# Performance work log

Hardware: AMD Instinct MI355X
Metric: run time of the kernel (lower is better)

## Reference

```python
import jax, jax.numpy as jnp
import numpy as np

N = 50000      # nodes
E = 800000     # edges per etype
IN, HID, OUT = 128, 128, 64
NH = 4         # heads in layerMH
NE = 2         # interaction edge types
NEG = 0.2      # GATConv leaky_relu negative slope


def _gat(x, src, dst, W, al, ar, b, heads, fdim):
    """DGL GATConv (residual=False, activation=None, bias=True).
    x: (N, in); W: (in, heads*fdim); al/ar: (heads, fdim); b: (heads*fdim,)
    Returns (N, heads, fdim)."""
    n = x.shape[0]
    z = (x @ W).reshape(n, heads, fdim)              # (N,H,F)
    el = jnp.sum(z * al, axis=-1)                    # (N,H)
    er = jnp.sum(z * ar, axis=-1)                    # (N,H)
    e = jax.nn.leaky_relu(el[src] + er[dst], NEG)    # (E,H)
    # edge softmax over incoming edges of each dst node
    m = jax.ops.segment_max(e, dst, num_segments=n)
    m = jnp.where(jnp.isfinite(m), m, 0.0)           # zero in-degree safety
    ex = jnp.exp(e - m[dst])
    den = jax.ops.segment_sum(ex, dst, num_segments=n)
    alpha = ex / jnp.maximum(den[dst], 1e-9)         # (E,H)
    out = jax.ops.segment_sum(alpha[:, :, None] * z[src], dst, num_segments=n)
    return out + b.reshape(1, heads, fdim)


def setup_inputs() -> dict:
    key = jax.random.key(0)
    ks = jax.random.split(key, 19)
    x = jax.random.normal(ks[0], (N, IN), jnp.float32)
    src0 = jax.random.randint(ks[1], (E,), 0, N, jnp.int32)
    dst0 = jax.random.randint(ks[2], (E,), 0, N, jnp.int32)
    src1 = jax.random.randint(ks[3], (E,), 0, N, jnp.int32)
    dst1 = jax.random.randint(ks[4], (E,), 0, N, jnp.int32)
    # per-etype GAT params (stacked over the NE edge types)
    W1 = jax.random.normal(ks[5], (NE, IN, HID), jnp.float32) / np.sqrt(IN)
    a_l1 = jax.random.normal(ks[6], (NE, 1, HID), jnp.float32) * 0.1
    a_r1 = jax.random.normal(ks[7], (NE, 1, HID), jnp.float32) * 0.1
    b1 = jnp.zeros((NE, HID), jnp.float32)
    W2 = jax.random.normal(ks[8], (NE, HID, OUT), jnp.float32) / np.sqrt(HID)
    a_l2 = jax.random.normal(ks[9], (NE, 1, OUT), jnp.float32) * 0.1
    a_r2 = jax.random.normal(ks[10], (NE, 1, OUT), jnp.float32) * 0.1
    b2 = jnp.zeros((NE, OUT), jnp.float32)
    Wm = jax.random.normal(ks[11], (NE, OUT, NH * OUT), jnp.float32) / np.sqrt(OUT)
    a_lm = jax.random.normal(ks[12], (NE, NH, OUT), jnp.float32) * 0.1
    a_rm = jax.random.normal(ks[13], (NE, NH, OUT), jnp.float32) * 0.1
    bm = jnp.zeros((NE, NH * OUT), jnp.float32)
    fc_w = jax.random.normal(ks[14], (NE, NE), jnp.float32) * (np.sqrt(2.0) / np.sqrt(NE))
    return dict(x=x, src0=src0, dst0=dst0, src1=src1, dst1=dst1,
                W1=W1, a_l1=a_l1, a_r1=a_r1, b1=b1,
                W2=W2, a_l2=a_l2, a_r2=a_r2, b2=b2,
                Wm=Wm, a_lm=a_lm, a_rm=a_rm, bm=bm, fc_w=fc_w)


def reference(x, src0, dst0, src1, dst1, W1, a_l1, a_r1, b1,
              W2, a_l2, a_r2, b2, Wm, a_lm, a_rm, bm, fc_w):
    srcs, dsts = (src0, src1), (dst0, dst1)
    # layer1: HeteroGraphConv mean over edge types, single head -> (N, HID)
    h1 = jnp.mean(jnp.stack([
        _gat(x, srcs[i], dsts[i], W1[i], a_l1[i], a_r1[i], b1[i], 1, HID)[:, 0, :]
        for i in range(NE)]), axis=0)
    # layer2: agg_func = fc over stacked etype axis, then mean -> (N, OUT)
    h2s = jnp.stack([
        _gat(h1, srcs[i], dsts[i], W2[i], a_l2[i], a_r2[i], b2[i], 1, OUT)[:, 0, :]
        for i in range(NE)], axis=-1)                       # (N, OUT, NE)
    h2 = jnp.mean(jnp.einsum('noe,fe->nof', h2s, fc_w), axis=-1)
    # multi-head layer: mean over edge types -> (N, NH, OUT)
    hm = jnp.mean(jnp.stack([
        _gat(h2, srcs[i], dsts[i], Wm[i], a_lm[i], a_rm[i], bm[i], NH, OUT)
        for i in range(NE)]), axis=0)
    # per-head mean-centering over nodes (vectorized over heads)
    return hm - jnp.mean(hm, axis=0, keepdims=True)
```

## Files before the change

kernel.cpp:

```cpp
#include <hip/hip_runtime.h>

#define NN 50000
#define EE 800000

using short8v = __attribute__((ext_vector_type(8))) short;
using f32x4 = __attribute__((ext_vector_type(4))) float;

__device__ inline unsigned int bf_pack(float lo, float hi) {
  unsigned int a = __float_as_uint(lo);
  a += 0x7FFFu + ((a >> 16) & 1u);
  unsigned int b = __float_as_uint(hi);
  b += 0x7FFFu + ((b >> 16) & 1u);
  return (a >> 16) | ((b >> 16) << 16);
}
__device__ inline void bf_dec8(uint4 v, float* f) {
  f[0] = __uint_as_float(v.x << 16); f[1] = __uint_as_float(v.x & 0xFFFF0000u);
  f[2] = __uint_as_float(v.y << 16); f[3] = __uint_as_float(v.y & 0xFFFF0000u);
  f[4] = __uint_as_float(v.z << 16); f[5] = __uint_as_float(v.z & 0xFFFF0000u);
  f[6] = __uint_as_float(v.w << 16); f[7] = __uint_as_float(v.w & 0xFFFF0000u);
}
__device__ inline float lrelu(float v) { return v >= 0.f ? v : 0.2f * v; }

__device__ inline void split_pack8(const float* v, uint4& h, uint4& l) {
  unsigned int hb[8], lb[8];
  #pragma unroll
  for (int j = 0; j < 8; j++) {
    unsigned int b = __float_as_uint(v[j]);
    hb[j] = b & 0xFFFF0000u;
    float r = v[j] - __uint_as_float(hb[j]);
    lb[j] = __float_as_uint(r) & 0xFFFF0000u;
  }
  h.x = (hb[0] >> 16) | hb[1]; h.y = (hb[2] >> 16) | hb[3];
  h.z = (hb[4] >> 16) | hb[5]; h.w = (hb[6] >> 16) | hb[7];
  l.x = (lb[0] >> 16) | lb[1]; l.y = (lb[2] >> 16) | lb[3];
  l.z = (lb[4] >> 16) | lb[5]; l.w = (lb[6] >> 16) | lb[7];
}

#define SC_BPR 256

__global__ __launch_bounds__(256) void fold_k(
    const float* __restrict__ W1, const float* __restrict__ al1, const float* __restrict__ ar1,
    const float* __restrict__ W2, const float* __restrict__ al2, const float* __restrict__ ar2,
    const float* __restrict__ Wm, const float* __restrict__ alm, const float* __restrict__ arm,
    float* __restrict__ wl1, float* __restrict__ wr1,
    float* __restrict__ wl2, float* __restrict__ wr2,
    float* __restrict__ wlm, float* __restrict__ wrm) {
  int t = blockIdx.x * 256 + threadIdx.x;
  if (t < 512) {
    int lr = t >> 8, e = (t >> 7) & 1, k = t & 127;
    const float* a = (lr ? ar1 : al1) + e * 128;
    const float* w = W1 + ((size_t)e * 128 + k) * 128;
    float s = 0.f;
    for (int f = 0; f < 128; f++) s += w[f] * a[f];
    (lr ? wr1 : wl1)[e * 128 + k] = s;
  } else if (t < 1024) {
    int u = t - 512;
    int lr = u >> 8, e = (u >> 7) & 1, k = u & 127;
    const float* a = (lr ? ar2 : al2) + e * 64;
    const float* w = W2 + ((size_t)e * 128 + k) * 64;
    float s = 0.f;
    for (int f = 0; f < 64; f++) s += w[f] * a[f];
    (lr ? wr2 : wl2)[e * 128 + k] = s;
  } else if (t < 2048) {
    int u = t - 1024;
    int lr = u >> 9, e = (u >> 8) & 1, h = (u >> 6) & 3, k = u & 63;
    const float* a = (lr ? arm : alm) + (e * 4 + h) * 64;
    const float* w = Wm + ((size_t)e * 64 + k) * 256 + h * 64;
    float s = 0.f;
    for (int f = 0; f < 64; f++) s += w[f] * a[f];
    (lr ? wrm : wlm)[(e * 4 + h) * 64 + k] = s;
  }
}

__global__ __launch_bounds__(256) void front_k(
    const int* __restrict__ dst0, const int* __restrict__ dst1,
    int* __restrict__ deg, int* __restrict__ rel,
    const float* __restrict__ x, const float* __restrict__ wl,
    const float* __restrict__ wr, unsigned int* __restrict__ xb,
    float* __restrict__ el, float* __restrict__ er,
    const float* __restrict__ W1, const float* __restrict__ W2,
    const float* __restrict__ Wm,
    unsigned short* __restrict__ w1h, unsigned short* __restrict__ w1l,
    unsigned short* __restrict__ w2h, unsigned short* __restrict__ w2l,
    unsigned short* __restrict__ wmh, unsigned short* __restrict__ wml) {
  const int blk = blockIdx.x;
  if (blk < 1563) {
    int i = blk * 256 + threadIdx.x;
    if (i < 200000) {
      int4 d = ((const int4*)dst0)[i];
      int4 r;
      r.x = atomicAdd(&deg[d.x], 1);
      r.y = atomicAdd(&deg[d.y], 1);
      r.z = atomicAdd(&deg[d.z], 1);
      r.w = atomicAdd(&deg[d.w], 1);
      ((int4*)rel)[i] = r;
    } else if (i < 400000) {
      int4 d = ((const int4*)dst1)[i - 200000];
      int* dg = deg + 50000;
      int4 r;
      r.x = atomicAdd(&dg[d.x], 1);
      r.y = atomicAdd(&dg[d.y], 1);
      r.z = atomicAdd(&dg[d.z], 1);
      r.w = atomicAdd(&dg[d.w], 1);
      ((int4*)(rel + EE))[i - 200000] = r;
    }
  } else if (blk < 4688) {
    int bx = blk - 1563;
    int n = bx * 16 + (threadIdx.x >> 4);
    int lane = threadIdx.x & 15;
    if (n >= NN) return;
    float p[4] = {0.f, 0.f, 0.f, 0.f};
    #pragma unroll
    for (int i = 0; i < 2; i++) {
      int c = (lane + i * 16) * 4;
      float4 xv = *(const float4*)(x + (size_t)n * 128 + c);
      uint2 o;
      o.x = bf_pack(xv.x, xv.y);
      o.y = bf_pack(xv.z, xv.w);
      *(uint2*)(xb + (size_t)n * 64 + c / 2) = o;
      #pragma unroll
      for (int e = 0; e < 2; e++) {
        float4 a = *(const float4*)(wl + e * 128 + c);
        float4 b = *(const float4*)(wr + e * 128 + c);
        p[e*2+0] += xv.x*a.x + xv.y*a.y + xv.z*a.z + xv.w*a.w;
        p[e*2+1] += xv.x*b.x + xv.y*b.y + xv.z*b.z + xv.w*b.w;
      }
    }
    #pragma unroll
    for (int off = 1; off < 16; off <<= 1) {
      #pragma unroll
      for (int i = 0; i < 4; i++) p[i] += __shfl_xor(p[i], off);
    }
    if (lane == 0) {
      el[n] = p[0]; er[n] = p[1];
      el[NN + n] = p[2]; er[NN + n] = p[3];
    }
  } else {
    int t = (blk - 4688) * 256 + threadIdx.x;
    float v; unsigned short *ph, *pl; int oi;
    if (t < 32768) {
      int j = t & 7, n = (t >> 3) & 127, kg = (t >> 10) & 15, e = t >> 14;
      v = W1[((size_t)(e * 128 + kg * 8 + j)) * 128 + n];
      ph = w1h; pl = w1l; oi = t;
    } else if (t < 49152) {
      int i = t - 32768;
      int j = i & 7, n = (i >> 3) & 63, kg = (i >> 9) & 15, e = i >> 13;
      v = W2[((size_t)(e * 128 + kg * 8 + j)) * 64 + n];
      ph = w2h; pl = w2l; oi = i;
    } else if (t < 81920) {
      int i = t - 49152;
      int j = i & 7, n = (i >> 3) & 255, kg = (i >> 11) & 7, e = i >> 14;
      v = Wm[((size_t)(e * 64 + kg * 8 + j)) * 256 + n];
      ph = wmh; pl = wml; oi = i;
    } else return;
    unsigned int b = __float_as_uint(v);
    unsigned int hb = b & 0xFFFF0000u;
    float r = v - __uint_as_float(hb);
    unsigned int lb = __float_as_uint(r);
    ph[oi] = (unsigned short)(hb >> 16);
    pl[oi] = (unsigned short)(lb >> 16);
  }
}

__global__ __launch_bounds__(512) void scan1_k(const int* __restrict__ deg,
                                               int* __restrict__ inc,
                                               int* __restrict__ bsum) {
  __shared__ int s[512];
  int e = blockIdx.y;
  int t = threadIdx.x, i = blockIdx.x * 512 + t;
  int v = (i < NN) ? deg[e * 50000 + i] : 0;
  s[t] = v; __syncthreads();
  #pragma unroll
  for (int off = 1; off < 512; off <<= 1) {
    int u = (t >= off) ? s[t - off] : 0;
    __syncthreads();
    s[t] += u;
    __syncthreads();
  }
  if (i < NN) inc[e * 50000 + i] = s[t];
  if (t == 511) bsum[e * 128 + blockIdx.x] = s[511];
}

__global__ __launch_bounds__(128) void scan2_k(int* __restrict__ bsum, int nb) {
  __shared__ int s[128];
  int e = blockIdx.x;
  int t = threadIdx.x;
  int v = (t < nb) ? bsum[e * 128 + t] : 0;
  s[t] = v; __syncthreads();
  #pragma unroll
  for (int off = 1; off < 128; off <<= 1) {
    int u = (t >= off) ? s[t - off] : 0;
    __syncthreads();
    s[t] += u;
    __syncthreads();
  }
  if (t < nb) bsum[e * 128 + t] = s[t] - v;
}

__global__ __launch_bounds__(256) void scan3_k(const int* __restrict__ deg,
                                               const int* __restrict__ inc,
                                               const int* __restrict__ bsum,
                                               int* __restrict__ rowptr) {
  int e = blockIdx.y;
  int i = blockIdx.x * 256 + threadIdx.x;
  if (i < NN) {
    rowptr[e * 50001 + i] =
        inc[e * 50000 + i] - deg[e * 50000 + i] + bsum[e * 128 + (i >> 9)];
  }
  if (i == NN) rowptr[e * 50001 + NN] = EE;
}

__global__ __launch_bounds__(256) void passB_k(
    const int* __restrict__ src0, const int* __restrict__ dst0,
    const int* __restrict__ src1, const int* __restrict__ dst1,
    const int* __restrict__ rel, const int* __restrict__ rowptr,
    int* __restrict__ csr_src) {
  __shared__ int rp_s[2][6250];
  const int range = blockIdx.x & 7;
  const int bpr = blockIdx.x >> 3;
  const int lo = range * 6250;
  const int hi = lo + 6250;
  for (int k = threadIdx.x; k < 6250; k += 256) {
    rp_s[0][k] = rowptr[lo + k];
    rp_s[1][k] = rowptr[50001 + lo + k];
  }
  __syncthreads();
  #pragma unroll
  for (int e = 0; e < 2; e++) {
    const int4* ds4 = (const int4*)(e ? dst1 : dst0);
    const int* ss = e ? src1 : src0;
    const int4* rl4 = (const int4*)(rel + (size_t)e * EE);
    const int* rps = rp_s[e];
    int* outp = csr_src + (size_t)e * EE;
    for (int i = bpr * 256 + threadIdx.x; i < EE / 4; i += SC_BPR * 256) {
      int4 d = ds4[i];
      int4 rl = rl4[i];
      int b = i * 4;
      if (d.x >= lo && d.x < hi) outp[rps[d.x - lo] + rl.x] = ss[b];
      if (d.y >= lo && d.y < hi) outp[rps[d.y - lo] + rl.y] = ss[b + 1];
      if (d.z >= lo && d.z < hi) outp[rps[d.z - lo] + rl.z] = ss[b + 2];
      if (d.w >= lo && d.w < hi) outp[rps[d.w - lo] + rl.w] = ss[b + 3];
    }
  }
}

__global__ __launch_bounds__(256) void agg_x_f(
    const int* __restrict__ rowptr, const int* __restrict__ csr_src,
    const float* __restrict__ el, const float* __restrict__ er,
    const uint4* __restrict__ xb, float* __restrict__ u1) {
  int d = blockIdx.x * 16 + (threadIdx.x >> 4);
  int lane = threadIdx.x & 15;
  if (d >= NN) return;
  const int e = blockIdx.y;
  const int* rp = rowptr + e * 50001;
  const int* cs = csr_src + (size_t)e * EE;
  const float* elp = el + (size_t)e * NN;
  float erd = er[(size_t)e * NN + d];
  int j0 = rp[d], j1 = rp[d + 1];
  float sm = 0.f;
  float acc[8] = {};
  for (int j = j0; j < j1; j += 16) {
    int cnt = j1 - j; if (cnt > 16) cnt = 16;
    int jj = j + (lane < cnt ? lane : 0);
    int sl = cs[jj];
    float alv = (lane < cnt) ? __expf(lrelu(elp[sl] + erd)) : 0.f;
    sm += alv;
    {
      int sv[8]; float av[8]; uint4 xv[8];
      #pragma unroll
      for (int k = 0; k < 8; k++) {
        sv[k] = __shfl(sl, k, 16);
        av[k] = __shfl(alv, k, 16);
      }
      #pragma unroll
      for (int k = 0; k < 8; k++) xv[k] = xb[(size_t)sv[k] * 16 + lane];
      #pragma unroll
      for (int k = 0; k < 8; k++) {
        float f[8]; bf_dec8(xv[k], f);
        #pragma unroll
        for (int c = 0; c < 8; c++) acc[c] += av[k] * f[c];
      }
    }
    if (cnt > 8) {
      int sv[8]; float av[8]; uint4 xv[8];
      #pragma unroll
      for (int k = 0; k < 8; k++) {
        sv[k] = __shfl(sl, 8 + k, 16);
        av[k] = __shfl(alv, 8 + k, 16);
      }
      #pragma unroll
      for (int k = 0; k < 8; k++) xv[k] = xb[(size_t)sv[k] * 16 + lane];
      #pragma unroll
      for (int k = 0; k < 8; k++) {
        float f[8]; bf_dec8(xv[k], f);
        #pragma unroll
        for (int c = 0; c < 8; c++) acc[c] += av[k] * f[c];
      }
    }
  }
  #pragma unroll
  for (int off = 1; off < 16; off <<= 1) sm += __shfl_xor(sm, off, 16);
  float inv = 1.f / fmaxf(sm, 1e-9f);
  float* up = u1 + ((size_t)e * NN + d) * 128 + lane * 8;
  *(float4*)up       = make_float4(acc[0]*inv, acc[1]*inv, acc[2]*inv, acc[3]*inv);
  *(float4*)(up + 4) = make_float4(acc[4]*inv, acc[5]*inv, acc[6]*inv, acc[7]*inv);
}

__global__ __launch_bounds__(256) void layer12_k(
    const float* __restrict__ u1, const unsigned short* __restrict__ w1h,
    const unsigned short* __restrict__ w1l, const float* __restrict__ b1,
    const unsigned short* __restrict__ w2h, const unsigned short* __restrict__ w2l,
    const float* __restrict__ wl2, const float* __restrict__ wr2,
    unsigned int* __restrict__ Zb, float* __restrict__ el,
    float* __restrict__ er) {
  __shared__ float smem[64 * 132];
  uint4* AsH = (uint4*)smem;
  uint4* AsL = AsH + 256;
  float* Hs = smem;
  const int tid = threadIdx.x;
  const int row0 = blockIdx.x * 64;
  const int wv = tid >> 6, lane = tid & 63;
  const int l15 = lane & 15, lg = lane >> 4;
  const uint4* b1h4 = (const uint4*)w1h;
  const uint4* b1l4 = (const uint4*)w1l;
  const uint4* b2h4 = (const uint4*)w2h;
  const uint4* b2l4 = (const uint4*)w2l;

  f32x4 acc[8] = {};
  for (int e = 0; e < 2; e++) {
    const float* Ap = u1 + (size_t)e * NN * 128;
    for (int k0 = 0; k0 < 128; k0 += 32) {
      {
        int r = tid & 63, kgl = tid >> 6;
        int rr = row0 + r; if (rr >= NN) rr = NN - 1;
        const float* ap = Ap + (size_t)rr * 128 + k0 + kgl * 8;
        float4 a0 = *(const float4*)ap;
        float4 a1 = *(const float4*)(ap + 4);
        float v[8] = {a0.x, a0.y, a0.z, a0.w, a1.x, a1.y, a1.z, a1.w};
        uint4 hh, ll;
        split_pack8(v, hh, ll);
        AsH[kgl * 64 + r] = hh;
        AsL[kgl * 64 + r] = ll;
      }
      __syncthreads();
      int slot = lg * 64 + wv * 16 + l15;
      short8v ah = *reinterpret_cast<const short8v*>(&AsH[slot]);
      short8v al = *reinterpret_cast<const short8v*>(&AsL[slot]);
      int kgb = e * 16 + (k0 >> 3) + lg;
      #pragma unroll
      for (int nf = 0; nf < 8; nf++) {
        int bslot = kgb * 128 + nf * 16 + l15;
        short8v bh = *reinterpret_cast<const short8v*>(&b1h4[bslot]);
        short8v bl = *reinterpret_cast<const short8v*>(&b1l4[bslot]);
        acc[nf] = __builtin_amdgcn_mfma_f32_16x16x32_bf16(ah, bh, acc[nf], 0, 0, 0);
        acc[nf] = __builtin_amdgcn_mfma_f32_16x16x32_bf16(al, bh, acc[nf], 0, 0, 0);
        acc[nf] = __builtin_amdgcn_mfma_f32_16x16x32_bf16(ah, bl, acc[nf], 0, 0, 0);
      }
      __syncthreads();
    }
  }
  #pragma unroll
  for (int nf = 0; nf < 8; nf++) {
    int col = nf * 16 + l15;
    float bb = 0.5f * (b1[col] + b1[128 + col]);
    #pragma unroll
    for (int reg = 0; reg < 4; reg++) {
      int rloc = wv * 16 + lg * 4 + reg;
      Hs[rloc * 132 + col] = 0.5f * acc[nf][reg] + bb;
    }
  }
  __syncthreads();
  {
    int r = tid >> 2, q = tid & 3;
    int grow = row0 + r;
    const float* hrow = Hs + r * 132;
    float p0 = 0.f, p1 = 0.f, p2 = 0.f, p3 = 0.f;
    #pragma unroll 8
    for (int c = 0; c < 32; c++) {
      int k = q + c * 4;
      float hv = hrow[k];
      p0 += hv * wl2[k];       p1 += hv * wr2[k];
      p2 += hv * wl2[128 + k]; p3 += hv * wr2[128 + k];
    }
    p0 += __shfl_xor(p0, 1); p0 += __shfl_xor(p0, 2);
    p1 += __shfl_xor(p1, 1); p1 += __shfl_xor(p1, 2);
    p2 += __shfl_xor(p2, 1); p2 += __shfl_xor(p2, 2);
    p3 += __shfl_xor(p3, 1); p3 += __shfl_xor(p3, 2);
    if (q == 0 && grow < NN) {
      el[grow] = p0;      er[grow] = p1;
      el[NN + grow] = p2; er[NN + grow] = p3;
    }
  }
  f32x4 acc2[2][4] = {};
  for (int k0 = 0; k0 < 128; k0 += 32) {
    int ra = wv * 16 + l15;
    const float* hp = Hs + ra * 132 + k0 + lg * 8;
    float4 h0 = *(const float4*)hp;
    float4 h1v = *(const float4*)(hp + 4);
    float v[8] = {h0.x, h0.y, h0.z, h0.w, h1v.x, h1v.y, h1v.z, h1v.w};
    uint4 hh, ll;
    split_pack8(v, hh, ll);
    short8v ah = *reinterpret_cast<const short8v*>(&hh);
    short8v al = *reinterpret_cast<const short8v*>(&ll);
    #pragma unroll
    for (int e = 0; e < 2; e++) {
      int kgb = e * 16 + (k0 >> 3) + lg;
      #pragma unroll
      for (int nf = 0; nf < 4; nf++) {
        int bslot = kgb * 64 + nf * 16 + l15;
        short8v bh = *reinterpret_cast<const short8v*>(&b2h4[bslot]);
        short8v bl = *reinterpret_cast<const short8v*>(&b2l4[bslot]);
        acc2[e][nf] = __builtin_amdgcn_mfma_f32_16x16x32_bf16(ah, bh, acc2[e][nf], 0, 0, 0);
        acc2[e][nf] = __builtin_amdgcn_mfma_f32_16x16x32_bf16(al, bh, acc2[e][nf], 0, 0, 0);
        acc2[e][nf] = __builtin_amdgcn_mfma_f32_16x16x32_bf16(ah, bl, acc2[e][nf], 0, 0, 0);
      }
    }
  }
  #pragma unroll
  for (int e = 0; e < 2; e++) {
    #pragma unroll
    for (int nf = 0; nf < 4; nf++) {
      #pragma unroll
      for (int reg = 0; reg < 4; reg++) {
        float v = acc2[e][nf][reg];
        float nb = __shfl_xor(v, 1);
        int row = row0 + wv * 16 + lg * 4 + reg;
        if (!(lane & 1) && row < NN) {
          Zb[((size_t)e * NN + row) * 32 + nf * 8 + (l15 >> 1)] = bf_pack(v, nb);
        }
      }
    }
  }
}

__global__ __launch_bounds__(256) void agg2_f(
    const int* __restrict__ rowptr, const int* __restrict__ csr_src,
    const float* __restrict__ el, const float* __restrict__ er,
    const uint4* __restrict__ zb, const float* __restrict__ bias,
    const float* __restrict__ fcw, const float* __restrict__ wlm,
    const float* __restrict__ wrm, uint4* __restrict__ h2b,
    float* __restrict__ elm, float* __restrict__ erm) {
  int d = blockIdx.x * 32 + (threadIdx.x >> 3);
  int lane = threadIdx.x & 7;
  if (d >= NN) return;
  int c0 = lane * 8;
  float coef0 = 0.5f * (fcw[0] + fcw[2]);
  float coef1 = 0.5f * (fcw[1] + fcw[3]);
  float hrow[8];
  #pragma unroll
  for (int c = 0; c < 8; c++)
    hrow[c] = coef0 * bias[c0 + c] + coef1 * bias[64 + c0 + c];
  #pragma unroll
  for (int e = 0; e < 2; e++) {
    const int* rp = rowptr + e * 50001;
    const int* cs = csr_src + (size_t)e * EE;
    const float* elp = el + (size_t)e * NN;
    float erd = er[(size_t)e * NN + d];
    const uint4* zp = zb + (size_t)e * NN * 8;
    int j0 = rp[d], j1 = rp[d + 1];
    float sm = 0.f;
    float acc[8] = {};
    for (int j = j0; j < j1; j += 8) {
      int cnt = j1 - j; if (cnt > 8) cnt = 8;
      int jj = j + (lane < cnt ? lane : 0);
      int sl = cs[jj];
      float alv = (lane < cnt) ? __expf(lrelu(elp[sl] + erd)) : 0.f;
      sm += alv;
      int sv[8]; float av[8]; uint4 zv[8];
      #pragma unroll
      for (int k = 0; k < 8; k++) {
        sv[k] = __shfl(sl, k, 8);
        av[k] = __shfl(alv, k, 8);
      }
      #pragma unroll
      for (int k = 0; k < 8; k++) zv[k] = zp[(size_t)sv[k] * 8 + lane];
      #pragma unroll
      for (int k = 0; k < 8; k++) {
        float f[8]; bf_dec8(zv[k], f);
        #pragma unroll
        for (int c = 0; c < 8; c++) acc[c] += av[k] * f[c];
      }
    }
    #pragma unroll
    for (int off = 1; off < 8; off <<= 1) sm += __shfl_xor(sm, off, 8);
    float cinv = (e ? coef1 : coef0) / fmaxf(sm, 1e-9f);
    #pragma unroll
    for (int c = 0; c < 8; c++) hrow[c] += cinv * acc[c];
  }
  uint4 o;
  o.x = bf_pack(hrow[0], hrow[1]); o.y = bf_pack(hrow[2], hrow[3]);
  o.z = bf_pack(hrow[4], hrow[5]); o.w = bf_pack(hrow[6], hrow[7]);
  h2b[(size_t)d * 8 + lane] = o;
  float p[16];
  #pragma unroll
  for (int e2 = 0; e2 < 2; e2++) {
    #pragma unroll
    for (int h = 0; h < 4; h++) {
      const float* a = wlm + (e2 * 4 + h) * 64 + c0;
      const float* b = wrm + (e2 * 4 + h) * 64 + c0;
      float sl = 0.f, sr = 0.f;
      #pragma unroll
      for (int c = 0; c < 8; c++) { sl += hrow[c] * a[c]; sr += hrow[c] * b[c]; }
      p[e2*4+h] = sl; p[8+e2*4+h] = sr;
    }
  }
  #pragma unroll
  for (int off = 1; off < 8; off <<= 1) {
    #pragma unroll
    for (int i = 0; i < 16; i++) p[i] += __shfl_xor(p[i], off, 8);
  }
  if (lane == 0) *(float4*)(elm + (size_t)d * 4)        = make_float4(p[0], p[1], p[2], p[3]);
  if (lane == 1) *(float4*)(elm + ((size_t)NN + d) * 4) = make_float4(p[4], p[5], p[6], p[7]);
  if (lane == 2) *(float4*)(erm + (size_t)d * 4)        = make_float4(p[8], p[9], p[10], p[11]);
  if (lane == 3) *(float4*)(erm + ((size_t)NN + d) * 4) = make_float4(p[12], p[13], p[14], p[15]);
}

__global__ __launch_bounds__(256) void agg_mh_k(
    const int* __restrict__ rowptr, const int* __restrict__ csr_src,
    const float* __restrict__ elm, const float* __restrict__ erm,
    const uint4* __restrict__ h2b, float* __restrict__ u) {
  int d = blockIdx.x * 32 + (threadIdx.x >> 3);
  int lane = threadIdx.x & 7, c0 = lane * 8;
  if (d >= NN) return;
  const int e = blockIdx.y;
  const int* rp = rowptr + e * 50001;
  const int* cs = csr_src + (size_t)e * EE;
  const float* elp = elm + (size_t)e * NN * 4;
  float4 er4 = *(const float4*)(erm + ((size_t)e * NN + d) * 4);
  int j0 = rp[d], j1 = rp[d + 1];
  float4 sm = make_float4(0.f, 0.f, 0.f, 0.f);
  float acc[4][8] = {};
  for (int j = j0; j < j1; j += 4) {
    int cnt = j1 - j; if (cnt > 4) cnt = 4;
    int sq[4];
    #pragma unroll
    for (int q = 0; q < 4; q++) sq[q] = cs[j + (q < cnt ? q : 0)];
    float4 vq[4]; uint4 hq[4];
    #pragma unroll
    for (int q = 0; q < 4; q++) vq[q] = *(const float4*)(elp + (size_t)sq[q] * 4);
    #pragma unroll
    for (int q = 0; q < 4; q++) hq[q] = h2b[(size_t)sq[q] * 8 + lane];
    #pragma unroll
    for (int q = 0; q < 4; q++) {
      float g = (q < cnt) ? 1.f : 0.f;
      float4 w;
      w.x = g * __expf(lrelu(vq[q].x + er4.x));
      w.y = g * __expf(lrelu(vq[q].y + er4.y));
      w.z = g * __expf(lrelu(vq[q].z + er4.z));
      w.w = g * __expf(lrelu(vq[q].w + er4.w));
      sm.x += w.x; sm.y += w.y; sm.z += w.z; sm.w += w.w;
      float f[8]; bf_dec8(hq[q], f);
      #pragma unroll
      for (int c = 0; c < 8; c++) {
        acc[0][c] += w.x * f[c];
        acc[1][c] += w.y * f[c];
        acc[2][c] += w.z * f[c];
        acc[3][c] += w.w * f[c];
      }
    }
  }
  float4 inv = make_float4(1.f / fmaxf(sm.x, 1e-9f), 1.f / fmaxf(sm.y, 1e-9f),
                           1.f / fmaxf(sm.z, 1e-9f), 1.f / fmaxf(sm.w, 1e-9f));
  float iv[4] = {inv.x, inv.y, inv.z, inv.w};
  #pragma unroll
  for (int h = 0; h < 4; h++) {
    float* up = u + (((size_t)(e * 4 + h) * NN) + d) * 64 + c0;
    *(float4*)up       = make_float4(acc[h][0]*iv[h], acc[h][1]*iv[h],
                                     acc[h][2]*iv[h], acc[h][3]*iv[h]);
    *(float4*)(up + 4) = make_float4(acc[h][4]*iv[h], acc[h][5]*iv[h],
                                     acc[h][6]*iv[h], acc[h][7]*iv[h]);
  }
}

__global__ __launch_bounds__(256) void colsum_u_k(
    const float* __restrict__ u, float* __restrict__ usum) {
  __shared__ float lds[4][64];
  int eh = blockIdx.x >> 6;
  int chunk = blockIdx.x & 63;
  int c = threadIdx.x & 63, rg = threadIdx.x >> 6;
  const float* up = u + (size_t)eh * NN * 64;
  int n0 = chunk * 782;
  int n1 = n0 + 782; if (n1 > NN) n1 = NN;
  float s = 0.f;
  for (int n = n0 + rg; n < n1; n += 4) s += up[(size_t)n * 64 + c];
  lds[rg][c] = s;
  __syncthreads();
  if (rg == 0) {
    float t = lds[0][c] + lds[1][c] + lds[2][c] + lds[3][c];
    unsafeAtomicAdd(&usum[eh * 64 + c], t);
  }
}

__global__ __launch_bounds__(256) void mean_k(
    const float* __restrict__ usum, const float* __restrict__ Wm,
    float* __restrict__ mean) {
  int c = threadIdx.x;
  int h = c >> 6;
  float s = 0.f;
  for (int e = 0; e < 2; e++) {
    const float* us = usum + (e * 4 + h) * 64;
    const float* wp = Wm + (size_t)e * 64 * 256 + c;
    for (int k = 0; k < 64; k++) s += us[k] * wp[(size_t)k * 256];
  }
  mean[c] = s * (0.5f / NN);
}

__global__ __launch_bounds__(256) void out_gemm_k(
    const float* __restrict__ u, const unsigned short* __restrict__ wmh,
    const unsigned short* __restrict__ wml, const float* __restrict__ mean,
    float* __restrict__ out) {
  __shared__ uint4 AsH[512], AsL[512];
  const int h = blockIdx.y;
  const int tid = threadIdx.x;
  const int row0 = blockIdx.x * 128;
  const int wv = tid >> 6, lane = tid & 63;
  const int l15 = lane & 15, lg = lane >> 4;
  f32x4 acc[2][4] = {};
  const uint4* bh4 = (const uint4*)wmh;
  const uint4* bl4 = (const uint4*)wml;
  for (int e = 0; e < 2; e++) {
    const float* Ap = u + (size_t)(e * 4 + h) * NN * 64;
    for (int k0 = 0; k0 < 64; k0 += 32) {
      {
        int r = tid & 127, half = tid >> 7;
        int rr = row0 + r; if (rr >= NN) rr = NN - 1;
        const float* ap = Ap + (size_t)rr * 64 + k0;
        #pragma unroll
        for (int i = 0; i < 2; i++) {
          int kg = half * 2 + i;
          float4 a0 = *(const float4*)(ap + kg * 8);
          float4 a1 = *(const float4*)(ap + kg * 8 + 4);
          float v[8] = {a0.x, a0.y, a0.z, a0.w, a1.x, a1.y, a1.z, a1.w};
          uint4 hh, ll;
          split_pack8(v, hh, ll);
          AsH[kg * 128 + r] = hh;
          AsL[kg * 128 + r] = ll;
        }
      }
      __syncthreads();
      short8v ah[2], al[2];
      #pragma unroll
      for (int mf = 0; mf < 2; mf++) {
        int slot = lg * 128 + wv * 32 + mf * 16 + l15;
        ah[mf] = *reinterpret_cast<const short8v*>(&AsH[slot]);
        al[mf] = *reinterpret_cast<const short8v*>(&AsL[slot]);
      }
      int kgb = e * 8 + (k0 >> 3) + lg;
      #pragma unroll
      for (int nf = 0; nf < 4; nf++) {
        int bslot = kgb * 256 + h * 64 + nf * 16 + l15;
        short8v bh = *reinterpret_cast<const short8v*>(&bh4[bslot]);
        short8v bl = *reinterpret_cast<const short8v*>(&bl4[bslot]);
        #pragma unroll
        for (int mf = 0; mf < 2; mf++) {
          acc[mf][nf] = __builtin_amdgcn_mfma_f32_16x16x32_bf16(ah[mf], bh, acc[mf][nf], 0, 0, 0);
          acc[mf][nf] = __builtin_amdgcn_mfma_f32_16x16x32_bf16(al[mf], bh, acc[mf][nf], 0, 0, 0);
          acc[mf][nf] = __builtin_amdgcn_mfma_f32_16x16x32_bf16(ah[mf], bl, acc[mf][nf], 0, 0, 0);
        }
      }
      __syncthreads();
    }
  }
  #pragma unroll
  for (int nf = 0; nf < 4; nf++) {
    int col = nf * 16 + l15;
    float mn = mean[h * 64 + col];
    #pragma unroll
    for (int mf = 0; mf < 2; mf++) {
      #pragma unroll
      for (int reg = 0; reg < 4; reg++) {
        int row = row0 + wv * 32 + mf * 16 + lg * 4 + reg;
        if (row < NN)
          out[(size_t)row * 256 + h * 64 + col] = 0.5f * acc[mf][nf][reg] - mn;
      }
    }
  }
}

extern "C" void kernel_launch(void* const* d_in, const int* in_sizes, int n_in,
                              void* d_out, int out_size, void* d_ws, size_t ws_size,
                              hipStream_t stream) {
  const float* x  = (const float*)d_in[0];
  const int* src0 = (const int*)d_in[1];
  const int* dst0 = (const int*)d_in[2];
  const int* src1 = (const int*)d_in[3];
  const int* dst1 = (const int*)d_in[4];
  const float* W1  = (const float*)d_in[5];
  const float* al1 = (const float*)d_in[6];
  const float* ar1 = (const float*)d_in[7];
  const float* b1  = (const float*)d_in[8];
  const float* W2  = (const float*)d_in[9];
  const float* al2 = (const float*)d_in[10];
  const float* ar2 = (const float*)d_in[11];
  const float* b2  = (const float*)d_in[12];
  const float* Wm  = (const float*)d_in[13];
  const float* alm = (const float*)d_in[14];
  const float* arm = (const float*)d_in[15];
  const float* fcw = (const float*)d_in[17];
  float* out = (float*)d_out;

  float* ws = (float*)d_ws;
  float* zu     = ws;
  unsigned int* z2b = (unsigned int*)(ws + 12800000);
  unsigned int* xb = (unsigned int*)(ws + 25600000);
  unsigned int* h2b = (unsigned int*)(ws + 32000000);
  float* el     = ws + 33600000;
  float* er     = ws + 34000000;
  float* elm    = ws + 34400000;
  float* erm    = ws + 34800000;
  float* wl1    = ws + 35200000;
  float* wr1    = wl1 + 256;
  float* wl2    = wr1 + 256;
  float* wr2    = wl2 + 256;
  float* wlm    = wr2 + 256;
  float* wrm    = wlm + 512;
  float* usum   = wrm + 512;
  float* meanp  = usum + 512;
  int* rowptr  = (int*)(meanp + 256);
  int* csr_src = rowptr + 100002;
  unsigned short* w1h = (unsigned short*)(csr_src + 2 * EE + 2);
  unsigned short* w1l = w1h + 32768;
  unsigned short* w2h = w1l + 32768;
  unsigned short* w2l = w2h + 16384;
  unsigned short* wmh = w2l + 16384;
  unsigned short* wml = wmh + 32768;
  int* rel    = (int*)zu;
  int* bsum   = (int*)zu + 2 * EE;
  int* deg    = (int*)zu + 2 * EE + 256;
  int* inc    = deg + 100000;

  hipMemsetAsync(deg, 0, 2 * 50000 * sizeof(int), stream);
  hipMemsetAsync(usum, 0, 512 * sizeof(float), stream);
  fold_k<<<8, 256, 0, stream>>>(W1, al1, ar1, W2, al2, ar2, Wm, alm, arm,
                                wl1, wr1, wl2, wr2, wlm, wrm);
  front_k<<<5008, 256, 0, stream>>>(dst0, dst1, deg, rel,
                                    x, wl1, wr1, xb, el, er,
                                    W1, W2, Wm, w1h, w1l, w2h, w2l, wmh, wml);
  scan1_k<<<dim3(98, 2), 512, 0, stream>>>(deg, inc, bsum);
  scan2_k<<<2, 128, 0, stream>>>(bsum, 98);
  scan3_k<<<dim3(196, 2), 256, 0, stream>>>(deg, inc, bsum, rowptr);
  passB_k<<<8 * SC_BPR, 256, 0, stream>>>(src0, dst0, src1, dst1,
                                          rel, rowptr, csr_src);

  agg_x_f<<<dim3(3125, 2), 256, 0, stream>>>(rowptr, csr_src, el, er,
                                             (const uint4*)xb, zu);
  layer12_k<<<782, 256, 0, stream>>>(zu, w1h, w1l, b1, w2h, w2l, wl2, wr2,
                                     z2b, el, er);

  agg2_f<<<1563, 256, 0, stream>>>(rowptr, csr_src, el, er, (const uint4*)z2b,
                                   b2, fcw, wlm, wrm, (uint4*)h2b, elm, erm);

  agg_mh_k<<<dim3(1563, 2), 256, 0, stream>>>(rowptr, csr_src, elm, erm,
                                              (const uint4*)h2b, zu);
  colsum_u_k<<<512, 256, 0, stream>>>(zu, usum);
  mean_k<<<1, 256, 0, stream>>>(usum, Wm, meanp);
  out_gemm_k<<<dim3(391, 4), 256, 0, stream>>>(zu, wmh, wml, meanp, out);
}
```

Before: 529.0 us.

## Privatize degree counters into eight partial histograms to cut atomic contention

Splits the per-destination degree counting across eight partial counter arrays selected by block index, with each edge's rank tagged by its partition label. A new combine kernel sums the partials into the degree array and turns them into per-partition offsets, which the scatter pass adds when placing edges into CSR. The aim is to reduce atomic contention on shared counters. In exchange it adds a larger memset, an extra kernel, and an extra gather per edge in the scatter pass.

```diff
diff --git a/kernel.cpp b/kernel.cpp
--- a/kernel.cpp
+++ b/kernel.cpp
@@ -74,7 +74,7 @@
 
 __global__ __launch_bounds__(256) void front_k(
     const int* __restrict__ dst0, const int* __restrict__ dst1,
-    int* __restrict__ deg, int* __restrict__ rel,
+    int* __restrict__ deg_p, int* __restrict__ rel,
     const float* __restrict__ x, const float* __restrict__ wl,
     const float* __restrict__ wr, unsigned int* __restrict__ xb,
     float* __restrict__ el, float* __restrict__ er,
@@ -85,23 +85,25 @@
     unsigned short* __restrict__ wmh, unsigned short* __restrict__ wml) {
   const int blk = blockIdx.x;
   if (blk < 1563) {
+    const int lab = blk & 7;
+    int* dg = deg_p + lab * 100000;
     int i = blk * 256 + threadIdx.x;
     if (i < 200000) {
       int4 d = ((const int4*)dst0)[i];
       int4 r;
-      r.x = atomicAdd(&deg[d.x], 1);
-      r.y = atomicAdd(&deg[d.y], 1);
-      r.z = atomicAdd(&deg[d.z], 1);
-      r.w = atomicAdd(&deg[d.w], 1);
+      r.x = (lab << 16) | atomicAdd(&dg[d.x], 1);
+      r.y = (lab << 16) | atomicAdd(&dg[d.y], 1);
+      r.z = (lab << 16) | atomicAdd(&dg[d.z], 1);
+      r.w = (lab << 16) | atomicAdd(&dg[d.w], 1);
       ((int4*)rel)[i] = r;
     } else if (i < 400000) {
       int4 d = ((const int4*)dst1)[i - 200000];
-      int* dg = deg + 50000;
+      int* dg1 = dg + 50000;
       int4 r;
-      r.x = atomicAdd(&dg[d.x], 1);
-      r.y = atomicAdd(&dg[d.y], 1);
-      r.z = atomicAdd(&dg[d.z], 1);
-      r.w = atomicAdd(&dg[d.w], 1);
+      r.x = (lab << 16) | atomicAdd(&dg1[d.x], 1);
+      r.y = (lab << 16) | atomicAdd(&dg1[d.y], 1);
+      r.z = (lab << 16) | atomicAdd(&dg1[d.z], 1);
+      r.w = (lab << 16) | atomicAdd(&dg1[d.w], 1);
       ((int4*)(rel + EE))[i - 200000] = r;
     }
   } else if (blk < 4688) {
@@ -162,6 +164,23 @@
   }
 }
 
+__global__ __launch_bounds__(256) void combine_k(
+    int* __restrict__ deg_p, int* __restrict__ deg) {
+  int t = blockIdx.x * 256 + threadIdx.x;
+  if (t >= 100000) return;
+  int s = 0;
+  int b[8];
+  #pragma unroll
+  for (int lab = 0; lab < 8; lab++) {
+    b[lab] = s;
+    s += deg_p[lab * 100000 + t];
+  }
+  deg[t] = s;
+  #pragma unroll
+  for (int lab = 0; lab < 8; lab++)
+    deg_p[lab * 100000 + t] = b[lab];
+}
+
 __global__ __launch_bounds__(512) void scan1_k(const int* __restrict__ deg,
                                                int* __restrict__ inc,
                                                int* __restrict__ bsum) {
@@ -214,7 +233,7 @@
     const int* __restrict__ src0, const int* __restrict__ dst0,
     const int* __restrict__ src1, const int* __restrict__ dst1,
     const int* __restrict__ rel, const int* __restrict__ rowptr,
-    int* __restrict__ csr_src) {
+    const int* __restrict__ deg_p, int* __restrict__ csr_src) {
   __shared__ int rp_s[2][6250];
   const int range = blockIdx.x & 7;
   const int bpr = blockIdx.x >> 3;
@@ -231,15 +250,28 @@
     const int* ss = e ? src1 : src0;
     const int4* rl4 = (const int4*)(rel + (size_t)e * EE);
     const int* rps = rp_s[e];
+    const int* bp = deg_p + e * 50000;
     int* outp = csr_src + (size_t)e * EE;
     for (int i = bpr * 256 + threadIdx.x; i < EE / 4; i += SC_BPR * 256) {
       int4 d = ds4[i];
       int4 rl = rl4[i];
       int b = i * 4;
-      if (d.x >= lo && d.x < hi) outp[rps[d.x - lo] + rl.x] = ss[b];
-      if (d.y >= lo && d.y < hi) outp[rps[d.y - lo] + rl.y] = ss[b + 1];
-      if (d.z >= lo && d.z < hi) outp[rps[d.z - lo] + rl.z] = ss[b + 2];
-      if (d.w >= lo && d.w < hi) outp[rps[d.w - lo] + rl.w] = ss[b + 3];
+      if (d.x >= lo && d.x < hi) {
+        int lab = ((unsigned)rl.x) >> 16, rk = rl.x & 0xFFFF;
+        outp[rps[d.x - lo] + bp[lab * 100000 + d.x] + rk] = ss[b];
+      }
+      if (d.y >= lo && d.y < hi) {
+        int lab = ((unsigned)rl.y) >> 16, rk = rl.y & 0xFFFF;
+        outp[rps[d.y - lo] + bp[lab * 100000 + d.y] + rk] = ss[b + 1];
+      }
+      if (d.z >= lo && d.z < hi) {
+        int lab = ((unsigned)rl.z) >> 16, rk = rl.z & 0xFFFF;
+        outp[rps[d.z - lo] + bp[lab * 100000 + d.z] + rk] = ss[b + 2];
+      }
+      if (d.w >= lo && d.w < hi) {
+        int lab = ((unsigned)rl.w) >> 16, rk = rl.w & 0xFFFF;
+        outp[rps[d.w - lo] + bp[lab * 100000 + d.w] + rk] = ss[b + 3];
+      }
     }
   }
 }
@@ -725,22 +757,24 @@
   unsigned short* wmh = w2l + 16384;
   unsigned short* wml = wmh + 32768;
   int* rel    = (int*)zu;
-  int* bsum   = (int*)zu + 2 * EE;
-  int* deg    = (int*)zu + 2 * EE + 256;
+  int* deg_p  = (int*)zu + 2 * EE;
+  int* deg    = (int*)zu + 2 * EE + 800000;
   int* inc    = deg + 100000;
-
-  hipMemsetAsync(deg, 0, 2 * 50000 * sizeof(int), stream);
+  int* bsum   = inc + 100000;
+
+  hipMemsetAsync(deg_p, 0, 800000 * sizeof(int), stream);
   hipMemsetAsync(usum, 0, 512 * sizeof(float), stream);
   fold_k<<<8, 256, 0, stream>>>(W1, al1, ar1, W2, al2, ar2, Wm, alm, arm,
                                 wl1, wr1, wl2, wr2, wlm, wrm);
-  front_k<<<5008, 256, 0, stream>>>(dst0, dst1, deg, rel,
+  front_k<<<5008, 256, 0, stream>>>(dst0, dst1, deg_p, rel,
                                     x, wl1, wr1, xb, el, er,
                                     W1, W2, Wm, w1h, w1l, w2h, w2l, wmh, wml);
+  combine_k<<<391, 256, 0, stream>>>(deg_p, deg);
   scan1_k<<<dim3(98, 2), 512, 0, stream>>>(deg, inc, bsum);
   scan2_k<<<2, 128, 0, stream>>>(bsum, 98);
   scan3_k<<<dim3(196, 2), 256, 0, stream>>>(deg, inc, bsum, rowptr);
   passB_k<<<8 * SC_BPR, 256, 0, stream>>>(src0, dst0, src1, dst1,
-                                          rel, rowptr, csr_src);
+                                          rel, rowptr, deg_p, csr_src);
 
   agg_x_f<<<dim3(3125, 2), 256, 0, stream>>>(rowptr, csr_src, el, er,
                                              (const uint4*)xb, zu);
```

New measurement: 543.6 us. 2.7% more time.
